# Kernel tuning notes

Hardware: AMD Instinct MI355X
Metric: run time of the kernel (lower is better)

The kernel has to match this reference:

```python
import jax, jax.numpy as jnp
import numpy as np

B, S, E = 4, 2048, 768
H, D = 3, E // 3  # 3 heads of size emb_sz//3


def setup_inputs() -> dict:
    key = jax.random.key(0)
    ks = jax.random.split(key, 8)
    inp = {
        "inputs_for_keys": jax.random.normal(ks[0], (B, S, E), jnp.float32),
        "inputs_for_values": jax.random.normal(ks[1], (B, S, E), jnp.float32),
        "inputs_for_queries": jax.random.normal(ks[2], (B, S, E), jnp.float32),
        # stacked per-head projections: [H, E, D] (same math as 3 separate tensordots)
        "WK": jax.random.normal(ks[3], (H, E, D), jnp.float32) * 0.02,
        "WV": jax.random.normal(ks[4], (H, E, D), jnp.float32) * 0.02,
        "WQ": jax.random.normal(ks[5], (H, E, D), jnp.float32) * 0.02,
        "Wo": jax.random.normal(ks[6], (E, E), jnp.float32) * 0.02,
        "bo": jnp.zeros((E,), jnp.float32),
    }
    return inp


def reference(inputs_for_keys, inputs_for_values, inputs_for_queries, WK, WV, WQ, Wo, bo):
    # per-head projections: [B, H, S, D]
    K = jnp.einsum("bse,hed->bhsd", inputs_for_keys, WK)
    V = jnp.einsum("bse,hed->bhsd", inputs_for_values, WV)
    Q = jnp.einsum("bse,hed->bhsd", inputs_for_queries, WQ)

    Sk = K.shape[2]
    # NOTE: original scales by sqrt(window_size_keys), not sqrt(head_dim)
    scores = jnp.einsum("bhqd,bhkd->bhqk", Q, K) / np.sqrt(Sk).astype(np.float32)
    # strictly-upper-triangular -inf causal mask (use_mask=True)
    causal = jnp.tril(jnp.ones((Q.shape[2], Sk), dtype=bool))
    scores = jnp.where(causal, scores, -jnp.inf)

    probs = jax.nn.softmax(scores, axis=-1)
    Z = jnp.einsum("bhqk,bhkd->bhqd", probs, V)  # [B, H, S, D]
    # concat heads (order 1,2,3) -> [B, S, E]
    concat = Z.transpose(0, 2, 1, 3).reshape(Z.shape[0], Z.shape[2], -1)
    return concat @ Wo + bo
```

## Files before the change

kernel.cpp:

```cpp
#include <hip/hip_runtime.h>
#include <hip/hip_bf16.h>

#define Bq 4
#define Sq 2048
#define Eq 768
#define Hq 3
#define Dq 256
#define BHq (Bq*Hq)

typedef __hip_bfloat16 bf16;
typedef __attribute__((ext_vector_type(8))) short bf16x8;
typedef __attribute__((ext_vector_type(4))) float f32x4;

__device__ __forceinline__ f32x4 mfma16(bf16x8 a, bf16x8 b, f32x4 c) {
    return __builtin_amdgcn_mfma_f32_16x16x32_bf16(a, b, c, 0, 0, 0);
}

__device__ __forceinline__ short f2bf(float x) {
    bf16 b = __float2bfloat16(x);
    return *(short*)&b;
}

__device__ __forceinline__ float bf2f(short s) {
    bf16 b = *reinterpret_cast<bf16*>(&s);
    return __bfloat162float(b);
}

__device__ __forceinline__ bf16x8 cvt8(float4 a, float4 b) {
    bf16x8 r;
    r[0] = f2bf(a.x); r[1] = f2bf(a.y); r[2] = f2bf(a.z); r[3] = f2bf(a.w);
    r[4] = f2bf(b.x); r[5] = f2bf(b.y); r[6] = f2bf(b.z); r[7] = f2bf(b.w);
    return r;
}

__device__ __forceinline__ void gl2lds16(const bf16* g, bf16* l) {
    __builtin_amdgcn_global_load_lds(
        (const __attribute__((address_space(1))) unsigned int*)g,
        (__attribute__((address_space(3))) unsigned int*)l,
        16, 0, 0);
}

__global__ __launch_bounds__(256) void prep_kernel(
        const float* __restrict__ Xk, const float* __restrict__ Xv,
        const float* __restrict__ Xq, bf16* __restrict__ Xb,
        const float* __restrict__ WK, const float* __restrict__ WV,
        const float* __restrict__ WQ, const float* __restrict__ Wo,
        bf16* __restrict__ WtK, bf16* __restrict__ Wot) {
    const int blk = blockIdx.x;
    const int tid = threadIdx.x;

    if (blk < 9216) {
        const int t = blk / 3072;
        const int i = blk % 3072;
        const float* X = (t == 0) ? Xk : (t == 1) ? Xv : Xq;
        size_t idx = ((size_t)i * 256 + tid) * 8;
        float4 a = *(const float4*)&X[idx];
        float4 b = *(const float4*)&X[idx + 4];
        *(bf16x8*)&Xb[(size_t)t * ((size_t)Bq * Sq * Eq) + idx] = cvt8(a, b);
        return;
    }

    __shared__ float tile[32][33];
    const float* in;
    bf16* out;
    int R, C, bx, by;
    if (blk < 10944) {
        int r  = blk - 9216;
        int t  = r / 576;
        int rr = r % 576;
        int batch = rr / 192;
        int tl = rr % 192;
        bx = tl & 7; by = tl >> 3;
        R = Eq; C = Dq;
        const float* Wsrc = (t == 0) ? WK : (t == 1) ? WV : WQ;
        in  = Wsrc + (size_t)batch * R * C;
        out = WtK + (size_t)t * ((size_t)Hq * Eq * Dq) + (size_t)batch * R * C;
    } else {
        int rr = blk - 10944;
        bx = rr % 24; by = rr / 24;
        R = Eq; C = Eq;
        in  = Wo;
        out = Wot;
    }
    const int tx = tid & 31;
    const int ty = tid >> 5;
#pragma unroll
    for (int i = ty; i < 32; i += 8)
        tile[i][tx] = in[(size_t)(by * 32 + i) * C + bx * 32 + tx];
    __syncthreads();
#pragma unroll
    for (int i = ty; i < 32; i += 8)
        out[(size_t)(bx * 32 + i) * R + by * 32 + tx] = __float2bfloat16(tile[tx][i]);
}

__global__ __launch_bounds__(256) void proj_kernel(
        const bf16* __restrict__ Xb, const bf16* __restrict__ Wt,
        bf16* __restrict__ Kp, bf16* __restrict__ Vt, bf16* __restrict__ Qp) {
    const int sel = blockIdx.y;
    const int x   = blockIdx.x;
    const int xcd = x & 7;
    const int kk0 = x >> 3;
    const int mt  = xcd * 8 + (kk0 / 6);
    const int nt  = kk0 % 6;
    const bf16* X = Xb + (size_t)sel * ((size_t)Bq * Sq * Eq);
    const bf16* W = Wt + (size_t)sel * ((size_t)Hq * Eq * Dq);

    __shared__ struct {
        bf16 A[2][128 * 32];
        bf16 B[2][128 * 32];
    } sm;
    auto& As = sm.A;
    auto& Bs = sm.B;

    const int tid  = threadIdx.x;
    const int lane = tid & 63;
    const int w    = tid >> 6;
    const int quad = lane >> 4;
    const int l16  = lane & 15;
    const int wm   = (w & 1) * 64;
    const int wn   = (w >> 1) * 64;

    const int m0 = mt * 128;
    const int n0 = nt * 128;

    int srow[2], skc[2];
#pragma unroll
    for (int i = 0; i < 2; ++i) {
        int ci  = (w * 2 + i) * 64 + lane;
        srow[i] = ci >> 2;
        skc[i]  = (ci & 3) ^ ((srow[i] >> 1) & 3);
    }

#define STAGE(buf, k0)                                                        \
    {                                                                         \
        _Pragma("unroll")                                                     \
        for (int i = 0; i < 2; ++i) {                                         \
            gl2lds16(&X[(size_t)(m0 + srow[i]) * Eq + (k0) + skc[i] * 8],     \
                     &As[buf][(w * 2 + i) * 512]);                            \
            gl2lds16(&W[(size_t)(n0 + srow[i]) * Eq + (k0) + skc[i] * 8],     \
                     &Bs[buf][(w * 2 + i) * 512]);                            \
        }                                                                     \
    }

    STAGE(0, 0);
    __syncthreads();

    f32x4 acc[4][4] = {};

    for (int s = 0; s < 24; ++s) {
        if (s + 1 < 24) STAGE((s + 1) & 1, (s + 1) * 32);
        const bf16* A  = As[s & 1];
        const bf16* Bv = Bs[s & 1];
        bf16x8 af[4], bfr[4];
#pragma unroll
        for (int mi = 0; mi < 4; ++mi) {
            int row = wm + mi * 16 + l16;
            int c   = quad ^ ((row >> 1) & 3);
            af[mi]  = *(const bf16x8*)&A[row * 32 + c * 8];
        }
#pragma unroll
        for (int ni = 0; ni < 4; ++ni) {
            int row = wn + ni * 16 + l16;
            int c   = quad ^ ((row >> 1) & 3);
            bfr[ni] = *(const bf16x8*)&Bv[row * 32 + c * 8];
        }
#pragma unroll
        for (int mi = 0; mi < 4; ++mi)
#pragma unroll
            for (int ni = 0; ni < 4; ++ni)
                acc[mi][ni] = mfma16(af[mi], bfr[ni], acc[mi][ni]);
        __syncthreads();
    }
#undef STAGE

    bf16* ct = (bf16*)&sm;
    const int b  = m0 / Sq;
    const int s0 = m0 % Sq;
    const int h  = n0 >> 8;
    const int d0 = n0 & 255;
    const int bh = b * Hq + h;

    if (sel == 1) {
#pragma unroll
        for (int mi = 0; mi < 4; ++mi)
#pragma unroll
            for (int ni = 0; ni < 4; ++ni)
#pragma unroll
                for (int r = 0; r < 4; ++r) {
                    int row = wn + ni * 16 + l16;
                    int col = wm + mi * 16 + quad * 4 + r;
                    ct[row * 128 + (((col >> 3) ^ (row & 15)) * 8) + (col & 7)] =
                        __float2bfloat16(acc[mi][ni][r]);
                }
    } else {
#pragma unroll
        for (int mi = 0; mi < 4; ++mi)
#pragma unroll
            for (int ni = 0; ni < 4; ++ni)
#pragma unroll
                for (int r = 0; r < 4; ++r) {
                    int row = wm + mi * 16 + quad * 4 + r;
                    int col = wn + ni * 16 + l16;
                    ct[row * 128 + (((col >> 3) ^ (row & 15)) * 8) + (col & 7)] =
                        __float2bfloat16(acc[mi][ni][r]);
                }
    }
    __syncthreads();
    {
        const int rr = tid >> 4;
        const int c  = tid & 15;
#pragma unroll
        for (int p = 0; p < 8; ++p) {
            int r  = p * 16 + rr;
            int cp = c ^ (r & 15);
            bf16x8 v = *(const bf16x8*)&ct[r * 128 + cp * 8];
            if (sel == 1)
                *(bf16x8*)&Vt[(size_t)(bh * Dq + d0 + r) * Sq + s0 + c * 8] = v;
            else if (sel == 0)
                *(bf16x8*)&Kp[(size_t)(bh * Sq + s0 + r) * Dq + d0 + c * 8] = v;
            else
                *(bf16x8*)&Qp[(size_t)(bh * Sq + s0 + r) * Dq + d0 + c * 8] = v;
        }
    }
}

__global__ __launch_bounds__(256, 2) void attn_kernel(
        const bf16* __restrict__ Qp, const bf16* __restrict__ Kp,
        const bf16* __restrict__ Vt, bf16* __restrict__ Z,
        bf16* __restrict__ Opart, float* __restrict__ lpart) {
    __shared__ bf16 Ks[64 * 256];
    __shared__ bf16 Vs[256 * 64];
    __shared__ bf16 Pl[4 * 16 * 64];

    const float SCALE = 0.022097086912079608f;

    const int id    = blockIdx.x;
    const int lane8 = id & 7;
    const int j     = id >> 3;
    const int W     = lane8 * 120 + j;
    const int bh    = W / 80;
    const int w80   = W % 80;
    int g8 = 0;
    if (w80 >= 8)  g8 = 1;
    if (w80 >= 24) g8 = 2;
    if (w80 >= 48) g8 = 3;
    const int rem   = w80 - 4 * g8 * (g8 + 1);
    const int qb    = g8 * 8 + rem / (g8 + 1);
    const int chunk = rem % (g8 + 1);
    const int t0    = chunk * 8;
    const int t1    = min(t0 + 8, qb + 1);
    const bool single = (qb < 8);

    const int tid  = threadIdx.x;
    const int lane = tid & 63;
    const int w    = tid >> 6;
    const int quad = lane >> 4;
    const int l16  = lane & 15;
    const int q0   = qb * 64 + w * 16;

    bf16x8 qf[8];
    {
        const bf16* Qbase = Qp + (size_t)(bh * Sq + q0 + l16) * Dq;
#pragma unroll
        for (int c = 0; c < 8; ++c)
            qf[c] = *(const bf16x8*)&Qbase[c * 32 + quad * 8];
    }

    const bf16* Kbh = Kp + (size_t)bh * Sq * Dq;
    const bf16* Vbh = Vt + (size_t)bh * Dq * Sq;

    f32x4 o[16] = {};
    float lsum[4] = {0.0f, 0.0f, 0.0f, 0.0f};

    for (int t = t0; t < t1; ++t) {
        const int k0 = t * 64;

        bf16x8 kreg[8], vreg[8];
#pragma unroll
        for (int p = 0; p < 8; ++p) {
            int c = p * 256 + tid;
            int row = c >> 5, cc = c & 31;
            kreg[p] = *(const bf16x8*)&Kbh[(size_t)(k0 + row) * Dq + cc * 8];
        }
#pragma unroll
        for (int p = 0; p < 8; ++p) {
            int c = p * 256 + tid;
            int row = c >> 3, cc = c & 7;
            vreg[p] = *(const bf16x8*)&Vbh[(size_t)row * Sq + k0 + cc * 8];
        }

        __syncthreads();
#pragma unroll
        for (int p = 0; p < 8; ++p) {
            int c = p * 256 + tid;
            int row = c >> 5, cc = c & 31;
            *(bf16x8*)&Ks[row * 256 + (cc ^ (row & 7)) * 8] = kreg[p];
        }
#pragma unroll
        for (int p = 0; p < 8; ++p) {
            int c = p * 256 + tid;
            int row = c >> 3, cc = c & 7;
            *(bf16x8*)&Vs[row * 64 + (cc ^ (row & 7)) * 8] = vreg[p];
        }
        __syncthreads();

        f32x4 sf[4] = {};
        __builtin_amdgcn_s_setprio(1);
#pragma unroll
        for (int c = 0; c < 8; ++c) {
            int cc = c * 4 + quad;
#pragma unroll
            for (int ni = 0; ni < 4; ++ni) {
                int key = ni * 16 + l16;
                bf16x8 kf = *(const bf16x8*)&Ks[key * 256 + (cc ^ (key & 7)) * 8];
                sf[ni] = mfma16(qf[c], kf, sf[ni]);
            }
        }
        __builtin_amdgcn_s_setprio(0);

        const bool diag = (t == qb);
#pragma unroll
        for (int ni = 0; ni < 4; ++ni) {
#pragma unroll
            for (int r = 0; r < 4; ++r) {
                float p = __expf(sf[ni][r] * SCALE);
                if (diag) {
                    int kg = k0 + ni * 16 + l16;
                    int qg = q0 + quad * 4 + r;
                    if (kg > qg) p = 0.0f;
                }
                lsum[r] += p;
                int row = quad * 4 + r;
                int col = ni * 16 + l16;
                int cc  = col >> 3;
                Pl[w * 1024 + row * 64 + (cc ^ (row & 7)) * 8 + (col & 7)] =
                    __float2bfloat16(p);
            }
        }

        __builtin_amdgcn_s_setprio(1);
#pragma unroll
        for (int c2 = 0; c2 < 2; ++c2) {
            int cc = c2 * 4 + quad;
            bf16x8 af = *(const bf16x8*)&Pl[w * 1024 + l16 * 64 + (cc ^ (l16 & 7)) * 8];
#pragma unroll
            for (int ni = 0; ni < 16; ++ni) {
                int d = ni * 16 + l16;
                bf16x8 vf = *(const bf16x8*)&Vs[d * 64 + (cc ^ (d & 7)) * 8];
                o[ni] = mfma16(af, vf, o[ni]);
            }
        }
        __builtin_amdgcn_s_setprio(0);
    }

#pragma unroll
    for (int off = 1; off < 16; off <<= 1)
#pragma unroll
        for (int r = 0; r < 4; ++r)
            lsum[r] += __shfl_xor(lsum[r], off);

    if (single) {
        const int b = bh / Hq, h = bh % Hq;
        float rinv[4];
#pragma unroll
        for (int r = 0; r < 4; ++r) rinv[r] = 1.0f / lsum[r];
#pragma unroll
        for (int ni = 0; ni < 16; ++ni) {
#pragma unroll
            for (int r = 0; r < 4; ++r) {
                int s = q0 + quad * 4 + r;
                int e = h * Dq + ni * 16 + l16;
                Z[(size_t)(b * Sq + s) * Eq + e] = __float2bfloat16(o[ni][r] * rinv[r]);
            }
        }
    } else {
        const int slot = bh * 80 + w80;
        bf16* Ob = Opart + (size_t)slot * (64 * 256);
#pragma unroll
        for (int ni = 0; ni < 16; ++ni) {
#pragma unroll
            for (int r = 0; r < 4; ++r) {
                int row = w * 16 + quad * 4 + r;
                int col = ni * 16 + l16;
                Ob[row * 256 + col] = __float2bfloat16(o[ni][r]);
            }
        }
        if (l16 == 0) {
#pragma unroll
            for (int r = 0; r < 4; ++r)
                lpart[(size_t)slot * 64 + w * 16 + quad * 4 + r] = lsum[r];
        }
    }
}

__global__ __launch_bounds__(256) void combine_kernel(
        const bf16* __restrict__ Opart, const float* __restrict__ lpart,
        bf16* __restrict__ Z) {
    const int qb = blockIdx.x;
    const int bh = blockIdx.y;
    if (qb < 8) return;
    const int g8 = qb >> 3;
    const int nch = g8 + 1;
    const int slot0 = bh * 80 + 4 * g8 * (g8 + 1) + (qb - g8 * 8) * (g8 + 1);

    const int tid = threadIdx.x;
    const int r   = tid >> 2;
    const int cs  = tid & 3;

    float l = 0.0f;
    for (int c = 0; c < nch; ++c)
        l += lpart[(size_t)(slot0 + c) * 64 + r];
    const float rinv = 1.0f / l;

    const int b = bh / Hq, h = bh % Hq;
    const int s = qb * 64 + r;
    bf16* zrow = Z + (size_t)(b * Sq + s) * Eq + h * Dq;

#pragma unroll
    for (int seg = 0; seg < 8; ++seg) {
        int col0 = cs * 64 + seg * 8;
        float acc[8] = {};
        for (int c = 0; c < nch; ++c) {
            bf16x8 v = *(const bf16x8*)&Opart[(size_t)(slot0 + c) * (64 * 256) + r * 256 + col0];
#pragma unroll
            for (int i = 0; i < 8; ++i) {
                short sv = v[i];
                acc[i] += bf2f(sv);
            }
        }
        bf16x8 outv;
#pragma unroll
        for (int i = 0; i < 8; ++i) outv[i] = f2bf(acc[i] * rinv);
        *(bf16x8*)&zrow[col0] = outv;
    }
}

__global__ __launch_bounds__(256) void outproj_kernel(
        const bf16* __restrict__ Z, const bf16* __restrict__ Wot,
        const float* __restrict__ bo, float* __restrict__ out) {
    const int x   = blockIdx.x;
    const int xcd = x & 7;
    const int kk0 = x >> 3;
    const int mt  = xcd * 8 + (kk0 / 6);
    const int nt  = kk0 % 6;

    __shared__ bf16 As[2][128 * 32];
    __shared__ bf16 Bs[2][128 * 32];

    const int tid  = threadIdx.x;
    const int lane = tid & 63;
    const int w    = tid >> 6;
    const int quad = lane >> 4;
    const int l16  = lane & 15;
    const int wm   = (w & 1) * 64;
    const int wn   = (w >> 1) * 64;

    const int m0 = mt * 128;
    const int n0 = nt * 128;

    int srow[2], skc[2];
#pragma unroll
    for (int i = 0; i < 2; ++i) {
        int ci  = (w * 2 + i) * 64 + lane;
        srow[i] = ci >> 2;
        skc[i]  = (ci & 3) ^ ((srow[i] >> 1) & 3);
    }

#define STAGE2(buf, k0)                                                       \
    {                                                                         \
        _Pragma("unroll")                                                     \
        for (int i = 0; i < 2; ++i) {                                         \
            gl2lds16(&Z[(size_t)(m0 + srow[i]) * Eq + (k0) + skc[i] * 8],     \
                     &As[buf][(w * 2 + i) * 512]);                            \
            gl2lds16(&Wot[(size_t)(n0 + srow[i]) * Eq + (k0) + skc[i] * 8],   \
                     &Bs[buf][(w * 2 + i) * 512]);                            \
        }                                                                     \
    }

    STAGE2(0, 0);
    __syncthreads();

    f32x4 acc[4][4] = {};

    for (int s = 0; s < 24; ++s) {
        if (s + 1 < 24) STAGE2((s + 1) & 1, (s + 1) * 32);
        const bf16* A  = As[s & 1];
        const bf16* Bv = Bs[s & 1];
        bf16x8 af[4], bfr[4];
#pragma unroll
        for (int mi = 0; mi < 4; ++mi) {
            int row = wm + mi * 16 + l16;
            int c   = quad ^ ((row >> 1) & 3);
            af[mi]  = *(const bf16x8*)&A[row * 32 + c * 8];
        }
#pragma unroll
        for (int ni = 0; ni < 4; ++ni) {
            int row = wn + ni * 16 + l16;
            int c   = quad ^ ((row >> 1) & 3);
            bfr[ni] = *(const bf16x8*)&Bv[row * 32 + c * 8];
        }
#pragma unroll
        for (int mi = 0; mi < 4; ++mi)
#pragma unroll
            for (int ni = 0; ni < 4; ++ni)
                acc[mi][ni] = mfma16(af[mi], bfr[ni], acc[mi][ni]);
        __syncthreads();
    }
#undef STAGE2

#pragma unroll
    for (int ni = 0; ni < 4; ++ni) {
        int n = n0 + wn + ni * 16 + l16;
        float bias = bo[n];
#pragma unroll
        for (int mi = 0; mi < 4; ++mi) {
#pragma unroll
            for (int r = 0; r < 4; ++r) {
                int m = m0 + wm + mi * 16 + quad * 4 + r;
                out[(size_t)m * Eq + n] = acc[mi][ni][r] + bias;
            }
        }
    }
}

extern "C" void kernel_launch(void* const* d_in, const int* in_sizes, int n_in,
                              void* d_out, int out_size, void* d_ws, size_t ws_size,
                              hipStream_t stream) {
    const float* Xk = (const float*)d_in[0];
    const float* Xv = (const float*)d_in[1];
    const float* Xq = (const float*)d_in[2];
    const float* WK = (const float*)d_in[3];
    const float* WV = (const float*)d_in[4];
    const float* WQ = (const float*)d_in[5];
    const float* Wo = (const float*)d_in[6];
    const float* bo = (const float*)d_in[7];
    float* out = (float*)d_out;

    bf16* ws = (bf16*)d_ws;
    const size_t WSZ  = (size_t)Hq * Eq * Dq;
    const size_t QKV  = (size_t)BHq * Sq * Dq;
    bf16* WtK = ws;
    bf16* WtO = WtK + 3 * WSZ;
    bf16* Qp  = WtO + (size_t)Eq * Eq;
    bf16* Kp  = Qp + QKV;
    bf16* Vt  = Kp + QKV;
    bf16* Zb  = Vt + QKV;
    bf16* Opart = Zb + QKV;
    bf16* Xb = Opart;
    float* lpart = (float*)(Opart + (size_t)3 * Bq * Sq * Eq);

    prep_kernel<<<11520, 256, 0, stream>>>(Xk, Xv, Xq, Xb, WK, WV, WQ, Wo, WtK, WtO);
    proj_kernel<<<dim3(384, 3), 256, 0, stream>>>(Xb, WtK, Kp, Vt, Qp);
    attn_kernel<<<960, 256, 0, stream>>>(Qp, Kp, Vt, Zb, Opart, lpart);
    combine_kernel<<<dim3(32, BHq), 256, 0, stream>>>(Opart, lpart, Zb);
    outproj_kernel<<<384, 256, 0, stream>>>(Zb, WtO, bo, out);
}
```

Before: 274.1 us.

## Enlarge projection GEMM tiles to 256x128 with 512-thread blocks; pad attention P buffer

```diff
diff --git a/kernel.cpp b/kernel.cpp
--- a/kernel.cpp
+++ b/kernel.cpp
@@ -93,20 +93,20 @@
         out[(size_t)(bx * 32 + i) * R + by * 32 + tx] = __float2bfloat16(tile[tx][i]);
 }
 
-__global__ __launch_bounds__(256) void proj_kernel(
+__global__ __launch_bounds__(512) void proj_kernel(
         const bf16* __restrict__ Xb, const bf16* __restrict__ Wt,
         bf16* __restrict__ Kp, bf16* __restrict__ Vt, bf16* __restrict__ Qp) {
     const int sel = blockIdx.y;
     const int x   = blockIdx.x;
     const int xcd = x & 7;
     const int kk0 = x >> 3;
-    const int mt  = xcd * 8 + (kk0 / 6);
+    const int mt  = xcd * 4 + (kk0 / 6);
     const int nt  = kk0 % 6;
     const bf16* X = Xb + (size_t)sel * ((size_t)Bq * Sq * Eq);
     const bf16* W = Wt + (size_t)sel * ((size_t)Hq * Eq * Dq);
 
     __shared__ struct {
-        bf16 A[2][128 * 32];
+        bf16 A[2][256 * 32];
         bf16 B[2][128 * 32];
     } sm;
     auto& As = sm.A;
@@ -117,29 +117,33 @@
     const int w    = tid >> 6;
     const int quad = lane >> 4;
     const int l16  = lane & 15;
-    const int wm   = (w & 1) * 64;
-    const int wn   = (w >> 1) * 64;
-
-    const int m0 = mt * 128;
+    const int wm   = (w & 3) * 64;
+    const int wn   = (w >> 2) * 64;
+
+    const int m0 = mt * 256;
     const int n0 = nt * 128;
 
-    int srow[2], skc[2];
+    int srowA[2], skcA[2], srowB, skcB;
 #pragma unroll
     for (int i = 0; i < 2; ++i) {
-        int ci  = (w * 2 + i) * 64 + lane;
-        srow[i] = ci >> 2;
-        skc[i]  = (ci & 3) ^ ((srow[i] >> 1) & 3);
+        int c8   = (w * 2 + i) * 64 + lane;
+        srowA[i] = c8 >> 2;
+        skcA[i]  = (c8 & 3) ^ ((srowA[i] >> 1) & 3);
+    }
+    {
+        int c8 = w * 64 + lane;
+        srowB  = c8 >> 2;
+        skcB   = (c8 & 3) ^ ((srowB >> 1) & 3);
     }
 
 #define STAGE(buf, k0)                                                        \
     {                                                                         \
         _Pragma("unroll")                                                     \
-        for (int i = 0; i < 2; ++i) {                                         \
-            gl2lds16(&X[(size_t)(m0 + srow[i]) * Eq + (k0) + skc[i] * 8],     \
+        for (int i = 0; i < 2; ++i)                                           \
+            gl2lds16(&X[(size_t)(m0 + srowA[i]) * Eq + (k0) + skcA[i] * 8],   \
                      &As[buf][(w * 2 + i) * 512]);                            \
-            gl2lds16(&W[(size_t)(n0 + srow[i]) * Eq + (k0) + skc[i] * 8],     \
-                     &Bs[buf][(w * 2 + i) * 512]);                            \
-        }                                                                     \
+        gl2lds16(&W[(size_t)(n0 + srowB) * Eq + (k0) + skcB * 8],             \
+                 &Bs[buf][w * 512]);                                          \
     }
 
     STAGE(0, 0);
@@ -179,48 +183,56 @@
     const int h  = n0 >> 8;
     const int d0 = n0 & 255;
     const int bh = b * Hq + h;
-
-    if (sel == 1) {
-#pragma unroll
-        for (int mi = 0; mi < 4; ++mi)
-#pragma unroll
-            for (int ni = 0; ni < 4; ++ni)
-#pragma unroll
-                for (int r = 0; r < 4; ++r) {
-                    int row = wn + ni * 16 + l16;
-                    int col = wm + mi * 16 + quad * 4 + r;
-                    ct[row * 128 + (((col >> 3) ^ (row & 15)) * 8) + (col & 7)] =
-                        __float2bfloat16(acc[mi][ni][r]);
-                }
-    } else {
-#pragma unroll
-        for (int mi = 0; mi < 4; ++mi)
-#pragma unroll
-            for (int ni = 0; ni < 4; ++ni)
-#pragma unroll
-                for (int r = 0; r < 4; ++r) {
-                    int row = wm + mi * 16 + quad * 4 + r;
-                    int col = wn + ni * 16 + l16;
-                    ct[row * 128 + (((col >> 3) ^ (row & 15)) * 8) + (col & 7)] =
-                        __float2bfloat16(acc[mi][ni][r]);
-                }
-    }
-    __syncthreads();
-    {
-        const int rr = tid >> 4;
-        const int c  = tid & 15;
-#pragma unroll
-        for (int p = 0; p < 8; ++p) {
-            int r  = p * 16 + rr;
-            int cp = c ^ (r & 15);
-            bf16x8 v = *(const bf16x8*)&ct[r * 128 + cp * 8];
-            if (sel == 1)
-                *(bf16x8*)&Vt[(size_t)(bh * Dq + d0 + r) * Sq + s0 + c * 8] = v;
-            else if (sel == 0)
-                *(bf16x8*)&Kp[(size_t)(bh * Sq + s0 + r) * Dq + d0 + c * 8] = v;
-            else
-                *(bf16x8*)&Qp[(size_t)(bh * Sq + s0 + r) * Dq + d0 + c * 8] = v;
-        }
+    const int whalf = (w >> 1) & 1;
+
+#pragma unroll
+    for (int hp = 0; hp < 2; ++hp) {
+        if (whalf == hp) {
+            const int wml = wm & 127;
+            if (sel == 1) {
+#pragma unroll
+                for (int mi = 0; mi < 4; ++mi)
+#pragma unroll
+                    for (int ni = 0; ni < 4; ++ni)
+#pragma unroll
+                        for (int r = 0; r < 4; ++r) {
+                            int row = wn + ni * 16 + l16;
+                            int col = wml + mi * 16 + quad * 4 + r;
+                            ct[row * 128 + (((col >> 3) ^ (row & 15)) * 8) + (col & 7)] =
+                                __float2bfloat16(acc[mi][ni][r]);
+                        }
+            } else {
+#pragma unroll
+                for (int mi = 0; mi < 4; ++mi)
+#pragma unroll
+                    for (int ni = 0; ni < 4; ++ni)
+#pragma unroll
+                        for (int r = 0; r < 4; ++r) {
+                            int row = wml + mi * 16 + quad * 4 + r;
+                            int col = wn + ni * 16 + l16;
+                            ct[row * 128 + (((col >> 3) ^ (row & 15)) * 8) + (col & 7)] =
+                                __float2bfloat16(acc[mi][ni][r]);
+                        }
+            }
+        }
+        __syncthreads();
+        {
+            const int rr = tid >> 4;
+            const int c  = tid & 15;
+#pragma unroll
+            for (int p = 0; p < 4; ++p) {
+                int r  = p * 32 + rr;
+                int cp = c ^ (r & 15);
+                bf16x8 v = *(const bf16x8*)&ct[r * 128 + cp * 8];
+                if (sel == 1)
+                    *(bf16x8*)&Vt[(size_t)(bh * Dq + d0 + r) * Sq + s0 + hp * 128 + c * 8] = v;
+                else if (sel == 0)
+                    *(bf16x8*)&Kp[(size_t)(bh * Sq + s0 + hp * 128 + r) * Dq + d0 + c * 8] = v;
+                else
+                    *(bf16x8*)&Qp[(size_t)(bh * Sq + s0 + hp * 128 + r) * Dq + d0 + c * 8] = v;
+            }
+        }
+        __syncthreads();
     }
 }
 
@@ -230,7 +242,7 @@
         bf16* __restrict__ Opart, float* __restrict__ lpart) {
     __shared__ bf16 Ks[64 * 256];
     __shared__ bf16 Vs[256 * 64];
-    __shared__ bf16 Pl[4 * 16 * 64];
+    __shared__ bf16 Pl[4 * 16 * 72];
 
     const float SCALE = 0.022097086912079608f;
 
@@ -330,10 +342,7 @@
                     if (kg > qg) p = 0.0f;
                 }
                 lsum[r] += p;
-                int row = quad * 4 + r;
-                int col = ni * 16 + l16;
-                int cc  = col >> 3;
-                Pl[w * 1024 + row * 64 + (cc ^ (row & 7)) * 8 + (col & 7)] =
+                Pl[w * 1152 + (quad * 4 + r) * 72 + ni * 16 + l16] =
                     __float2bfloat16(p);
             }
         }
@@ -342,7 +351,7 @@
 #pragma unroll
         for (int c2 = 0; c2 < 2; ++c2) {
             int cc = c2 * 4 + quad;
-            bf16x8 af = *(const bf16x8*)&Pl[w * 1024 + l16 * 64 + (cc ^ (l16 & 7)) * 8];
+            bf16x8 af = *(const bf16x8*)&Pl[w * 1152 + l16 * 72 + cc * 8];
 #pragma unroll
             for (int ni = 0; ni < 16; ++ni) {
                 int d = ni * 16 + l16;
@@ -435,16 +444,16 @@
     }
 }
 
-__global__ __launch_bounds__(256) void outproj_kernel(
+__global__ __launch_bounds__(512) void outproj_kernel(
         const bf16* __restrict__ Z, const bf16* __restrict__ Wot,
         const float* __restrict__ bo, float* __restrict__ out) {
     const int x   = blockIdx.x;
     const int xcd = x & 7;
     const int kk0 = x >> 3;
-    const int mt  = xcd * 8 + (kk0 / 6);
+    const int mt  = xcd * 4 + (kk0 / 6);
     const int nt  = kk0 % 6;
 
-    __shared__ bf16 As[2][128 * 32];
+    __shared__ bf16 As[2][256 * 32];
     __shared__ bf16 Bs[2][128 * 32];
 
     const int tid  = threadIdx.x;
@@ -452,29 +461,33 @@
     const int w    = tid >> 6;
     const int quad = lane >> 4;
     const int l16  = lane & 15;
-    const int wm   = (w & 1) * 64;
-    const int wn   = (w >> 1) * 64;
-
-    const int m0 = mt * 128;
+    const int wm   = (w & 3) * 64;
+    const int wn   = (w >> 2) * 64;
+
+    const int m0 = mt * 256;
     const int n0 = nt * 128;
 
-    int srow[2], skc[2];
+    int srowA[2], skcA[2], srowB, skcB;
 #pragma unroll
     for (int i = 0; i < 2; ++i) {
-        int ci  = (w * 2 + i) * 64 + lane;
-        srow[i] = ci >> 2;
-        skc[i]  = (ci & 3) ^ ((srow[i] >> 1) & 3);
+        int c8   = (w * 2 + i) * 64 + lane;
+        srowA[i] = c8 >> 2;
+        skcA[i]  = (c8 & 3) ^ ((srowA[i] >> 1) & 3);
+    }
+    {
+        int c8 = w * 64 + lane;
+        srowB  = c8 >> 2;
+        skcB   = (c8 & 3) ^ ((srowB >> 1) & 3);
     }
 
 #define STAGE2(buf, k0)                                                       \
     {                                                                         \
         _Pragma("unroll")                                                     \
-        for (int i = 0; i < 2; ++i) {                                         \
-            gl2lds16(&Z[(size_t)(m0 + srow[i]) * Eq + (k0) + skc[i] * 8],     \
+        for (int i = 0; i < 2; ++i)                                           \
+            gl2lds16(&Z[(size_t)(m0 + srowA[i]) * Eq + (k0) + skcA[i] * 8],   \
                      &As[buf][(w * 2 + i) * 512]);                            \
-            gl2lds16(&Wot[(size_t)(n0 + srow[i]) * Eq + (k0) + skc[i] * 8],   \
-                     &Bs[buf][(w * 2 + i) * 512]);                            \
-        }                                                                     \
+        gl2lds16(&Wot[(size_t)(n0 + srowB) * Eq + (k0) + skcB * 8],           \
+                 &Bs[buf][w * 512]);                                          \
     }
 
     STAGE2(0, 0);
@@ -550,8 +563,8 @@
     float* lpart = (float*)(Opart + (size_t)3 * Bq * Sq * Eq);
 
     prep_kernel<<<11520, 256, 0, stream>>>(Xk, Xv, Xq, Xb, WK, WV, WQ, Wo, WtK, WtO);
-    proj_kernel<<<dim3(384, 3), 256, 0, stream>>>(Xb, WtK, Kp, Vt, Qp);
+    proj_kernel<<<dim3(192, 3), 512, 0, stream>>>(Xb, WtK, Kp, Vt, Qp);
     attn_kernel<<<960, 256, 0, stream>>>(Qp, Kp, Vt, Zb, Opart, lpart);
     combine_kernel<<<dim3(32, BHq), 256, 0, stream>>>(Opart, lpart, Zb);
-    outproj_kernel<<<384, 256, 0, stream>>>(Zb, WtO, bo, out);
-}
+    outproj_kernel<<<192, 512, 0, stream>>>(Zb, WtO, bo, out);
+}
```

Result: no change. 279.0 us (+1.8%).

## Fuse split-K combine into attention via atomic last-block reduction; pad P tile

Applied to the files above, without the earlier changes.

```diff
diff --git a/kernel.cpp b/kernel.cpp
--- a/kernel.cpp
+++ b/kernel.cpp
@@ -45,11 +45,15 @@
         const float* __restrict__ Xq, bf16* __restrict__ Xb,
         const float* __restrict__ WK, const float* __restrict__ WV,
         const float* __restrict__ WQ, const float* __restrict__ Wo,
-        bf16* __restrict__ WtK, bf16* __restrict__ Wot) {
+        bf16* __restrict__ WtK, bf16* __restrict__ Wot,
+        int* __restrict__ cnt) {
     const int blk = blockIdx.x;
     const int tid = threadIdx.x;
 
     if (blk < 9216) {
+        if (blk == 0) {
+            for (int i = tid; i < BHq * 32; i += 256) cnt[i] = 0;
+        }
         const int t = blk / 3072;
         const int i = blk % 3072;
         const float* X = (t == 0) ? Xk : (t == 1) ? Xv : Xq;
@@ -227,10 +231,12 @@
 __global__ __launch_bounds__(256, 2) void attn_kernel(
         const bf16* __restrict__ Qp, const bf16* __restrict__ Kp,
         const bf16* __restrict__ Vt, bf16* __restrict__ Z,
-        bf16* __restrict__ Opart, float* __restrict__ lpart) {
+        bf16* __restrict__ Opart, float* __restrict__ lpart,
+        int* __restrict__ cnt) {
     __shared__ bf16 Ks[64 * 256];
     __shared__ bf16 Vs[256 * 64];
-    __shared__ bf16 Pl[4 * 16 * 64];
+    __shared__ bf16 Pl[4 * 16 * 72];
+    __shared__ int lastFlag;
 
     const float SCALE = 0.022097086912079608f;
 
@@ -330,10 +336,7 @@
                     if (kg > qg) p = 0.0f;
                 }
                 lsum[r] += p;
-                int row = quad * 4 + r;
-                int col = ni * 16 + l16;
-                int cc  = col >> 3;
-                Pl[w * 1024 + row * 64 + (cc ^ (row & 7)) * 8 + (col & 7)] =
+                Pl[w * 1152 + (quad * 4 + r) * 72 + ni * 16 + l16] =
                     __float2bfloat16(p);
             }
         }
@@ -342,7 +345,7 @@
 #pragma unroll
         for (int c2 = 0; c2 < 2; ++c2) {
             int cc = c2 * 4 + quad;
-            bf16x8 af = *(const bf16x8*)&Pl[w * 1024 + l16 * 64 + (cc ^ (l16 & 7)) * 8];
+            bf16x8 af = *(const bf16x8*)&Pl[w * 1152 + l16 * 72 + cc * 8];
 #pragma unroll
             for (int ni = 0; ni < 16; ++ni) {
                 int d = ni * 16 + l16;
@@ -373,7 +376,10 @@
                 Z[(size_t)(b * Sq + s) * Eq + e] = __float2bfloat16(o[ni][r] * rinv[r]);
             }
         }
-    } else {
+        return;
+    }
+
+    {
         const int slot = bh * 80 + w80;
         bf16* Ob = Opart + (size_t)slot * (64 * 256);
 #pragma unroll
@@ -391,47 +397,49 @@
                 lpart[(size_t)slot * 64 + w * 16 + quad * 4 + r] = lsum[r];
         }
     }
-}
-
-__global__ __launch_bounds__(256) void combine_kernel(
-        const bf16* __restrict__ Opart, const float* __restrict__ lpart,
-        bf16* __restrict__ Z) {
-    const int qb = blockIdx.x;
-    const int bh = blockIdx.y;
-    if (qb < 8) return;
-    const int g8 = qb >> 3;
-    const int nch = g8 + 1;
-    const int slot0 = bh * 80 + 4 * g8 * (g8 + 1) + (qb - g8 * 8) * (g8 + 1);
-
-    const int tid = threadIdx.x;
-    const int r   = tid >> 2;
-    const int cs  = tid & 3;
-
-    float l = 0.0f;
-    for (int c = 0; c < nch; ++c)
-        l += lpart[(size_t)(slot0 + c) * 64 + r];
-    const float rinv = 1.0f / l;
-
-    const int b = bh / Hq, h = bh % Hq;
-    const int s = qb * 64 + r;
-    bf16* zrow = Z + (size_t)(b * Sq + s) * Eq + h * Dq;
-
-#pragma unroll
-    for (int seg = 0; seg < 8; ++seg) {
-        int col0 = cs * 64 + seg * 8;
-        float acc[8] = {};
-        for (int c = 0; c < nch; ++c) {
-            bf16x8 v = *(const bf16x8*)&Opart[(size_t)(slot0 + c) * (64 * 256) + r * 256 + col0];
-#pragma unroll
-            for (int i = 0; i < 8; ++i) {
-                short sv = v[i];
-                acc[i] += bf2f(sv);
-            }
-        }
-        bf16x8 outv;
-#pragma unroll
-        for (int i = 0; i < 8; ++i) outv[i] = f2bf(acc[i] * rinv);
-        *(bf16x8*)&zrow[col0] = outv;
+
+    __threadfence();
+    __syncthreads();
+    if (tid == 0) {
+        int old = atomicAdd(&cnt[bh * 32 + qb], 1);
+        lastFlag = (old == g8);
+    }
+    __syncthreads();
+    if (!lastFlag) return;
+    __threadfence();
+
+    {
+        const int nch   = g8 + 1;
+        const int slot0 = bh * 80 + 4 * g8 * (g8 + 1) + (qb - g8 * 8) * (g8 + 1);
+        const int r  = tid >> 2;
+        const int cs = tid & 3;
+
+        float l = 0.0f;
+        for (int c = 0; c < nch; ++c)
+            l += lpart[(size_t)(slot0 + c) * 64 + r];
+        const float rinv = 1.0f / l;
+
+        const int b = bh / Hq, h = bh % Hq;
+        const int s = qb * 64 + r;
+        bf16* zrow = Z + (size_t)(b * Sq + s) * Eq + h * Dq;
+
+#pragma unroll
+        for (int seg = 0; seg < 8; ++seg) {
+            int col0 = cs * 64 + seg * 8;
+            float acc[8] = {};
+            for (int c = 0; c < nch; ++c) {
+                bf16x8 v = *(const bf16x8*)&Opart[(size_t)(slot0 + c) * (64 * 256) + r * 256 + col0];
+#pragma unroll
+                for (int i = 0; i < 8; ++i) {
+                    short sv = v[i];
+                    acc[i] += bf2f(sv);
+                }
+            }
+            bf16x8 outv;
+#pragma unroll
+            for (int i = 0; i < 8; ++i) outv[i] = f2bf(acc[i] * rinv);
+            *(bf16x8*)&zrow[col0] = outv;
+        }
     }
 }
 
@@ -548,10 +556,10 @@
     bf16* Opart = Zb + QKV;
     bf16* Xb = Opart;
     float* lpart = (float*)(Opart + (size_t)3 * Bq * Sq * Eq);
-
-    prep_kernel<<<11520, 256, 0, stream>>>(Xk, Xv, Xq, Xb, WK, WV, WQ, Wo, WtK, WtO);
+    int* cnt = (int*)(lpart + (size_t)960 * 64);
+
+    prep_kernel<<<11520, 256, 0, stream>>>(Xk, Xv, Xq, Xb, WK, WV, WQ, Wo, WtK, WtO, cnt);
     proj_kernel<<<dim3(384, 3), 256, 0, stream>>>(Xb, WtK, Kp, Vt, Qp);
-    attn_kernel<<<960, 256, 0, stream>>>(Qp, Kp, Vt, Zb, Opart, lpart);
-    combine_kernel<<<dim3(32, BHq), 256, 0, stream>>>(Opart, lpart, Zb);
+    attn_kernel<<<960, 256, 0, stream>>>(Qp, Kp, Vt, Zb, Opart, lpart, cnt);
     outproj_kernel<<<384, 256, 0, stream>>>(Zb, WtO, bo, out);
 }
```

New measurement: 445.2 us. 62.4% more time.
